# Optimization experiments

Measured on AMD Instinct MI355X. Metric: run time of the kernel, lower is better.

Reference implementation:

```python
import jax, jax.numpy as jnp
import numpy as np

NS = (128, 128, 128)       # ns_mesh
NODES = 4                  # interpolation_nodes (P3M, even -> floor-based indexing)
N_POINTS = 100000
N_CHANNELS = 8
BOX = 10.0


def _weights_p3m4(x):
    # x: (P, 3) relative offsets in [-1/2, 1/2]; returns (4, P, 3)
    x2 = x * x
    x3 = x * x2
    c = jnp.asarray(1.0 / 48.0, dtype=x.dtype)
    return jnp.stack([
        c * (1 - 6 * x + 12 * x2 - 8 * x3),
        c * (23 - 30 * x - 12 * x2 + 24 * x3),
        c * (23 + 30 * x - 12 * x2 - 24 * x3),
        c * (1 + 6 * x + 12 * x2 + 8 * x3),
    ])


def setup_inputs() -> dict:
    key = jax.random.key(0)
    k1, k2 = jax.random.split(key)
    positions = jax.random.uniform(k1, (N_POINTS, 3), dtype=jnp.float32) * BOX
    particle_weights = jax.random.normal(k2, (N_POINTS, N_CHANNELS), dtype=jnp.float32)
    cell = jnp.eye(3, dtype=jnp.float32) * BOX
    return {"positions": positions, "particle_weights": particle_weights, "cell": cell}


def reference(positions, particle_weights, cell):
    nx, ny, nz = NS
    ns_f = jnp.array(NS, dtype=positions.dtype)
    inv_cell = jnp.linalg.inv(cell)

    # --- compute_weights ---
    pos_rel = ns_f * (positions @ inv_cell)        # (P,3) mesh-scaled fractional coords
    idx0 = jnp.floor(pos_rel)                      # even nodes -> floor of position
    offsets = pos_rel - (idx0 + 0.5)               # in [-1/2, 1/2]
    w = _weights_p3m4(offsets)                     # (4, P, 3) per-axis 1d weights
    shifts = jnp.arange(1 - (NODES + 1) // 2, 1 + NODES // 2, dtype=jnp.int32)  # [-1,0,1,2]
    ns_i = jnp.array(NS, dtype=jnp.int32)
    idx = (idx0.astype(jnp.int32)[None] + shifts[:, None, None]) % ns_i  # (4,P,3) periodic
    xi, yi, zi = idx[..., 0], idx[..., 1], idx[..., 2]  # (4,P) each

    # 3D outer product of per-axis weights: (4,4,4,P)
    w3 = w[:, None, None, :, 0] * w[None, :, None, :, 1] * w[None, None, :, :, 2]
    # flattened mesh index per (i,j,k,point): (4,4,4,P)
    lin = (xi[:, None, None] * ny + yi[None, :, None]) * nz + zi[None, None, :]

    # --- points_to_mesh: scatter-add weighted charges onto mesh ---
    C = particle_weights.shape[1]
    vals = w3[..., None] * particle_weights        # (4,4,4,P,C)
    rho_flat = jnp.zeros((nx * ny * nz, C), dtype=positions.dtype)
    rho_flat = rho_flat.at[lin.reshape(-1)].add(vals.reshape(-1, C))

    # --- mesh_to_points: gather mesh values back to particle positions ---
    gathered = rho_flat[lin]                       # (4,4,4,P,C)
    out = jnp.sum(gathered * w3[..., None], axis=(0, 1, 2))  # (P,C)
    return out
```

## Files before the change

### kernel.cpp

```cpp
#include <hip/hip_runtime.h>

static constexpr int NXC   = 128;
static constexpr int NPTS  = 100000;
static constexpr int NCH   = 8;
static constexpr int TS    = 8;
static constexpr int NT    = 16;
static constexpr int NTILES = NT * NT * NT;
static constexpr int NT2   = 32;
static constexpr int NSB   = NT2 * NT2 * NT2;
static constexpr int SLOT2 = 24;
static constexpr int REC   = 20;
static constexpr int SLABCAP = 32;
static constexpr int AMAX  = 14 * SLABCAP;
static constexpr int OMAX2 = 8 * SLOT2;
static constexpr int NMAX  = 48;
static constexpr int NGRP  = 32;

__device__ __forceinline__ void axis_weights(float x, float w[4]) {
    float x2 = x * x, x3 = x2 * x;
    const float c = 1.0f / 48.0f;
    w[0] = c * (1.0f  - 6.0f  * x + 12.0f * x2 - 8.0f  * x3);
    w[1] = c * (23.0f - 30.0f * x - 12.0f * x2 + 24.0f * x3);
    w[2] = c * (23.0f + 30.0f * x - 12.0f * x2 - 24.0f * x3);
    w[3] = c * (1.0f  + 6.0f  * x + 12.0f * x2 + 8.0f  * x3);
}

__device__ __forceinline__ void mesh_coords(const float* __restrict__ pos,
                                            const float* __restrict__ cell,
                                            int p, float& rx, float& ry, float& rz) {
    float a = cell[0], b = cell[1], c = cell[2];
    float d = cell[3], e = cell[4], f = cell[5];
    float g = cell[6], h = cell[7], i9 = cell[8];
    float c00 = e * i9 - f * h, c01 = f * g - d * i9, c02 = d * h - e * g;
    float c10 = c * h - b * i9, c11 = a * i9 - c * g, c12 = b * g - a * h;
    float c20 = b * f - c * e,  c21 = c * d - a * f,  c22 = a * e - b * d;
    float det = a * c00 + b * c01 + c * c02;
    float s = 128.0f / det;
    float p0 = pos[p * 3 + 0], p1 = pos[p * 3 + 1], p2 = pos[p * 3 + 2];
    rx = s * (p0 * c00 + p1 * c01 + p2 * c02);
    ry = s * (p0 * c10 + p1 * c11 + p2 * c12);
    rz = s * (p0 * c20 + p1 * c21 + p2 * c22);
}

__global__ __launch_bounds__(256) void bin_k(const float* __restrict__ pos,
                                             const float* __restrict__ pw,
                                             const float* __restrict__ cell,
                                             int* __restrict__ cursor,
                                             int2* __restrict__ scp,
                                             float* __restrict__ srec) {
    int p = blockIdx.x * 256 + threadIdx.x;
    if (p >= NPTS) return;
    float rx, ry, rz;
    mesh_coords(pos, cell, p, rx, ry, rz);
    float fx = floorf(rx), fy = floorf(ry), fz = floorf(rz);
    int ix = ((int)fx) & (NXC - 1), iy = ((int)fy) & (NXC - 1), iz = ((int)fz) & (NXC - 1);
    int sb = ((ix >> 2) * NT2 + (iy >> 2)) * NT2 + (iz >> 2);
    int slot = atomicAdd(cursor + sb, 1);
    if (slot < SLOT2)
        scp[sb * SLOT2 + slot] = make_int2(ix | (iy << 10) | (iz << 20), p);
    float wx[4], wy[4], wz[4];
    axis_weights(rx - fx - 0.5f, wx);
    axis_weights(ry - fy - 0.5f, wy);
    axis_weights(rz - fz - 0.5f, wz);
    float4* r = reinterpret_cast<float4*>(srec) + (size_t)p * 5;
    r[0] = make_float4(wx[0], wx[1], wx[2], wx[3]);
    r[1] = make_float4(wy[0], wy[1], wy[2], wy[3]);
    r[2] = make_float4(wz[0], wz[1], wz[2], wz[3]);
    const float4* pw4 = reinterpret_cast<const float4*>(pw + (size_t)p * NCH);
    r[3] = pw4[0];
    r[4] = pw4[1];
}

__device__ __forceinline__ float corr4(float4 wp, float4 wq, int d) {
    float s0 = d == 0 ? wq.x : d == -1 ? wq.y : d == -2 ? wq.z : d == -3 ? wq.w : 0.0f;
    float s1 = d == 1 ? wq.x : d ==  0 ? wq.y : d == -1 ? wq.z : d == -2 ? wq.w : 0.0f;
    float s2 = d == 2 ? wq.x : d ==  1 ? wq.y : d ==  0 ? wq.z : d == -1 ? wq.w : 0.0f;
    float s3 = d == 3 ? wq.x : d ==  2 ? wq.y : d ==  1 ? wq.z : d ==  0 ? wq.w : 0.0f;
    return wp.x * s0 + wp.y * s1 + wp.z * s2 + wp.w * s3;
}

__global__ __launch_bounds__(256) void pair_k(const int* __restrict__ cursor,
                                              const int2* __restrict__ scp,
                                              const float* __restrict__ srec,
                                              float* __restrict__ out) {
    __shared__ int2 slab[AMAX];
    __shared__ int2 A12[AMAX];
    __shared__ int nlist[NGRP * NMAX];
    __shared__ int2 own[OMAX2];
    __shared__ int scnt[14];
    __shared__ int soff[15];
    __shared__ int ocnt;

    int b = blockIdx.x;
    int tx = b >> 8, ty = (b >> 4) & 15, tz = b & 15;
    int tid = threadIdx.x;
    int lane = tid & 63;

    if (tid < 14) scnt[tid] = 0;
    if (tid == 0) ocnt = 0;
    __syncthreads();

    {
        int crew = tid >> 2, cl = tid & 3;
        int ox = (crew >> 4) - 1, oy = ((crew >> 2) & 3) - 1, oz = (crew & 3) - 1;
        int sx = (2 * tx + ox) & (NT2 - 1);
        int sy = (2 * ty + oy) & (NT2 - 1);
        int sz = (2 * tz + oz) & (NT2 - 1);
        int sb = (sx * NT2 + sy) * NT2 + sz;
        int n0 = sb * SLOT2;
        int cn = min(cursor[sb], SLOT2);
        bool interior = ((unsigned)ox < 2u) && ((unsigned)oy < 2u) && ((unsigned)oz < 2u);
        int ob = 0;
        if (interior && cl == 0 && cn > 0) ob = atomicAdd(&ocnt, cn);
        ob = __shfl(ob, lane & 60, 64);
        if (interior) {
            for (int s = cl; s < cn; s += 4) own[ob + s] = scp[n0 + s];
        }
        int base_x = tx * TS - 3, base_y = ty * TS - 3, base_z = tz * TS - 3;
        for (int s0 = 0; s0 < cn; s0 += 4) {
            int s = s0 + cl;
            if (s < cn) {
                int2 e = scp[n0 + s];
                int c = e.x;
                int lcx = ((c & 1023) - base_x) & 127;
                int lcy = (((c >> 10) & 1023) - base_y) & 127;
                int lcz = (((c >> 20) & 1023) - base_z) & 127;
                if (lcx < 14 && lcy < 14 && lcz < 14) {
                    int slot = atomicAdd(&scnt[lcx], 1);
                    if (slot < SLABCAP)
                        slab[lcx * SLABCAP + slot] =
                            make_int2(lcy | (lcz << 5) | (lcx << 10), e.y);
                }
            }
        }
    }
    __syncthreads();
    int nown = ocnt;
    if (nown == 0) return;
    if (tid == 0) {
        int run = 0;
        #pragma unroll
        for (int s2 = 0; s2 < 14; ++s2) {
            soff[s2] = run;
            run += min(scnt[s2], SLABCAP);
        }
        soff[14] = run;
    }
    __syncthreads();
    for (int u = tid; u < AMAX; u += 256) {
        int s2 = u >> 5, i2 = u & (SLABCAP - 1);
        if (i2 < min(scnt[s2], SLABCAP)) A12[soff[s2] + i2] = slab[u];
    }
    __syncthreads();

    int sub = tid & 7, pg = tid >> 3;
    const float4* recs = reinterpret_cast<const float4*>(srec);
    int nbl = pg * NMAX;

    for (int p = pg; __any(p < nown); p += NGRP) {
        bool live = p < nown;
        int lpx = 0, lpyh = 0, lpzh = 0, jbeg = 0, span = 0, pid = 0;
        float4 pxw, pyw, pzw;
        if (live) {
            int2 oe = own[p];
            int pc = oe.x;
            pid = oe.y;
            lpx  = (pc & 1023) - tx * TS;
            lpyh = ((pc >> 10) & 1023) - ty * TS + 3;
            lpzh = ((pc >> 20) & 1023) - tz * TS + 3;
            jbeg = soff[lpx];
            span = soff[lpx + 7] - jbeg;
            const float4* r = recs + (size_t)pid * 5;
            pxw = r[0]; pyw = r[1]; pzw = r[2];
        }
        int creg = 0;
        for (int j0 = 0; __any(j0 < span); j0 += 8) {
            bool pass = (j0 + sub) < span;
            int a1 = 0, a2 = 0;
            if (pass) {
                int2 e = A12[jbeg + j0 + sub];
                a1 = e.x; a2 = e.y;
                int dy3 = (a1 & 31) - lpyh + 3;
                int dz3 = ((a1 >> 5) & 31) - lpzh + 3;
                pass = ((unsigned)dy3 <= 6u) && ((unsigned)dz3 <= 6u);
            }
            unsigned long long m = __ballot(pass);
            int mg = (int)(m >> (lane & 56)) & 255;
            if (pass) {
                int slot = creg + __popc(mg & ((1 << sub) - 1));
                if (slot < NMAX) {
                    int dxp3 = ((a1 >> 10) & 15) - lpx;
                    int dy3 = (a1 & 31) - lpyh + 3;
                    int dz3 = ((a1 >> 5) & 31) - lpzh + 3;
                    nlist[nbl + slot] = (a2 << 9) | (dxp3 << 6) | (dy3 << 3) | dz3;
                }
            }
            creg += __popc(mg);
        }
        int n = live ? min(creg, NMAX) : 0;
        float acc[8] = {0, 0, 0, 0, 0, 0, 0, 0};
        for (int s = sub; s < n; s += 8) {
            int ent = nlist[nbl + s];
            const float4* q = recs + (size_t)(ent >> 9) * 5;
            int dx = ((ent >> 6) & 7) - 3;
            int dy = ((ent >> 3) & 7) - 3;
            int dz = (ent & 7) - 3;
            float4 qxw = q[0], qyw = q[1], qzw = q[2];
            float S = corr4(pxw, qxw, dx) * corr4(pyw, qyw, dy) * corr4(pzw, qzw, dz);
            float4 ch0 = q[3], ch1 = q[4];
            acc[0] += S * ch0.x; acc[1] += S * ch0.y;
            acc[2] += S * ch0.z; acc[3] += S * ch0.w;
            acc[4] += S * ch1.x; acc[5] += S * ch1.y;
            acc[6] += S * ch1.z; acc[7] += S * ch1.w;
        }
        float t4[4];
        #pragma unroll
        for (int i = 0; i < 4; ++i) {
            float keep = (sub & 4) ? acc[i + 4] : acc[i];
            float send = (sub & 4) ? acc[i]     : acc[i + 4];
            t4[i] = keep + __shfl_xor(send, 4, 64);
        }
        float t2[2];
        #pragma unroll
        for (int i = 0; i < 2; ++i) {
            float keep = (sub & 2) ? t4[i + 2] : t4[i];
            float send = (sub & 2) ? t4[i]     : t4[i + 2];
            t2[i] = keep + __shfl_xor(send, 2, 64);
        }
        float keep1 = (sub & 1) ? t2[1] : t2[0];
        float send1 = (sub & 1) ? t2[0] : t2[1];
        float rres = keep1 + __shfl_xor(send1, 1, 64);
        if (live) out[(size_t)pid * NCH + sub] = rres;
    }
}

extern "C" void kernel_launch(void* const* d_in, const int* in_sizes, int n_in,
                              void* d_out, int out_size, void* d_ws, size_t ws_size,
                              hipStream_t stream) {
    const float* pos  = (const float*)d_in[0];
    const float* pw   = (const float*)d_in[1];
    const float* cell = (const float*)d_in[2];
    float* out = (float*)d_out;

    int*   cursor = (int*)d_ws;
    int2*  scp    = (int2*)(cursor + NSB);
    float* srec   = (float*)(scp + NSB * SLOT2);

    hipMemsetAsync(cursor, 0, NSB * sizeof(int), stream);

    int pblocks = (NPTS + 255) / 256;
    bin_k<<<pblocks, 256, 0, stream>>>(pos, pw, cell, cursor, scp, srec);
    pair_k<<<NTILES, 256, 0, stream>>>(cursor, scp, srec, out);
}
```

Baseline: 61.00 us.

## Assign one tile per wavefront and build neighbor slab with counting sort

Each 64-lane wavefront now processes its own tile, so a block handles four tiles and the grid shrinks fourfold. The per-x-slice slab-then-compact staging is replaced by a two-pass counting sort: count with shared atomics, take a shuffle prefix scan, then scatter straight into the compact array. Each lane scans a whole sub-box serially instead of four lanes sharing one, and capacity clamps (CMAX, OWNC) are added. This is meant to cut block-wide synchronisation and idle threads on sparse tiles. The cost is serial per-lane loops, two reads of each sub-box and possible truncation if a tile overflows the caps.

```diff
diff --git a/kernel.cpp b/kernel.cpp
--- a/kernel.cpp
+++ b/kernel.cpp
@@ -10,11 +10,9 @@
 static constexpr int NSB   = NT2 * NT2 * NT2;
 static constexpr int SLOT2 = 24;
 static constexpr int REC   = 20;
-static constexpr int SLABCAP = 32;
-static constexpr int AMAX  = 14 * SLABCAP;
-static constexpr int OMAX2 = 8 * SLOT2;
+static constexpr int CMAX  = 224;
+static constexpr int OWNC  = 96;
 static constexpr int NMAX  = 48;
-static constexpr int NGRP  = 32;
 
 __device__ __forceinline__ void axis_weights(float x, float w[4]) {
     float x2 = x * x, x3 = x2 * x;
@@ -83,81 +81,86 @@
                                               const int2* __restrict__ scp,
                                               const float* __restrict__ srec,
                                               float* __restrict__ out) {
-    __shared__ int2 slab[AMAX];
-    __shared__ int2 A12[AMAX];
-    __shared__ int nlist[NGRP * NMAX];
-    __shared__ int2 own[OMAX2];
-    __shared__ int scnt[14];
-    __shared__ int soff[15];
-    __shared__ int ocnt;
-
-    int b = blockIdx.x;
+    __shared__ int2 A12s[4][CMAX];
+    __shared__ int2 owns[4][OWNC];
+    __shared__ int  nlists[4][8 * NMAX];
+    __shared__ int  scnts[4][14];
+    __shared__ int  soffs[4][16];
+    __shared__ int  aoffs[4][14];
+    __shared__ int  ocnts[4];
+
+    int tid = threadIdx.x;
+    int wid = tid >> 6;
+    int lane = tid & 63;
+    int b = blockIdx.x * 4 + wid;
     int tx = b >> 8, ty = (b >> 4) & 15, tz = b & 15;
-    int tid = threadIdx.x;
-    int lane = tid & 63;
-
-    if (tid < 14) scnt[tid] = 0;
-    if (tid == 0) ocnt = 0;
-    __syncthreads();
-
-    {
-        int crew = tid >> 2, cl = tid & 3;
-        int ox = (crew >> 4) - 1, oy = ((crew >> 2) & 3) - 1, oz = (crew & 3) - 1;
-        int sx = (2 * tx + ox) & (NT2 - 1);
-        int sy = (2 * ty + oy) & (NT2 - 1);
-        int sz = (2 * tz + oz) & (NT2 - 1);
-        int sb = (sx * NT2 + sy) * NT2 + sz;
-        int n0 = sb * SLOT2;
-        int cn = min(cursor[sb], SLOT2);
-        bool interior = ((unsigned)ox < 2u) && ((unsigned)oy < 2u) && ((unsigned)oz < 2u);
-        int ob = 0;
-        if (interior && cl == 0 && cn > 0) ob = atomicAdd(&ocnt, cn);
-        ob = __shfl(ob, lane & 60, 64);
-        if (interior) {
-            for (int s = cl; s < cn; s += 4) own[ob + s] = scp[n0 + s];
-        }
-        int base_x = tx * TS - 3, base_y = ty * TS - 3, base_z = tz * TS - 3;
-        for (int s0 = 0; s0 < cn; s0 += 4) {
-            int s = s0 + cl;
-            if (s < cn) {
-                int2 e = scp[n0 + s];
-                int c = e.x;
-                int lcx = ((c & 1023) - base_x) & 127;
-                int lcy = (((c >> 10) & 1023) - base_y) & 127;
-                int lcz = (((c >> 20) & 1023) - base_z) & 127;
-                if (lcx < 14 && lcy < 14 && lcz < 14) {
-                    int slot = atomicAdd(&scnt[lcx], 1);
-                    if (slot < SLABCAP)
-                        slab[lcx * SLABCAP + slot] =
-                            make_int2(lcy | (lcz << 5) | (lcx << 10), e.y);
-                }
-            }
-        }
-    }
-    __syncthreads();
-    int nown = ocnt;
-    if (nown == 0) return;
-    if (tid == 0) {
-        int run = 0;
-        #pragma unroll
-        for (int s2 = 0; s2 < 14; ++s2) {
-            soff[s2] = run;
-            run += min(scnt[s2], SLABCAP);
-        }
-        soff[14] = run;
-    }
-    __syncthreads();
-    for (int u = tid; u < AMAX; u += 256) {
-        int s2 = u >> 5, i2 = u & (SLABCAP - 1);
-        if (i2 < min(scnt[s2], SLABCAP)) A12[soff[s2] + i2] = slab[u];
-    }
-    __syncthreads();
-
-    int sub = tid & 7, pg = tid >> 3;
+
+    int2* A12 = A12s[wid];
+    int2* own = owns[wid];
+    int*  nlist = nlists[wid];
+    int*  scnt = scnts[wid];
+    int*  soff = soffs[wid];
+    int*  aoff = aoffs[wid];
+
+    if (lane < 14) scnt[lane] = 0;
+    if (lane == 0) ocnts[wid] = 0;
+    __syncthreads();
+
+    int ox = (lane >> 4) - 1, oy = ((lane >> 2) & 3) - 1, oz = (lane & 3) - 1;
+    int sx = (2 * tx + ox) & (NT2 - 1);
+    int sy = (2 * ty + oy) & (NT2 - 1);
+    int sz = (2 * tz + oz) & (NT2 - 1);
+    int sb = (sx * NT2 + sy) * NT2 + sz;
+    int n0 = sb * SLOT2;
+    int cn = min(cursor[sb], SLOT2);
+    bool interior = ((unsigned)ox < 2u) && ((unsigned)oy < 2u) && ((unsigned)oz < 2u);
+    int base_x = tx * TS - 3, base_y = ty * TS - 3, base_z = tz * TS - 3;
+
+    int ob = 0;
+    if (interior && cn > 0) ob = atomicAdd(&ocnts[wid], cn);
+    for (int s = 0; s < cn; ++s) {
+        int2 e = scp[n0 + s];
+        if (interior && ob + s < OWNC) own[ob + s] = e;
+        int c = e.x;
+        int lcx = ((c & 1023) - base_x) & 127;
+        int lcy = (((c >> 10) & 1023) - base_y) & 127;
+        int lcz = (((c >> 20) & 1023) - base_z) & 127;
+        if (lcx < 14 && lcy < 14 && lcz < 14) atomicAdd(&scnt[lcx], 1);
+    }
+    __syncthreads();
+
+    int run = (lane < 14) ? scnt[lane] : 0;
+    #pragma unroll
+    for (int d = 1; d < 16; d <<= 1) {
+        int v = __shfl_up(run, d, 16);
+        if ((lane & 15) >= d) run += v;
+    }
+    if (lane == 0) soff[0] = 0;
+    if (lane < 14) soff[lane + 1] = min(run, CMAX);
+    __syncthreads();
+    if (lane < 14) aoff[lane] = soff[lane];
+    __syncthreads();
+
+    for (int s = 0; s < cn; ++s) {
+        int2 e = scp[n0 + s];
+        int c = e.x;
+        int lcx = ((c & 1023) - base_x) & 127;
+        int lcy = (((c >> 10) & 1023) - base_y) & 127;
+        int lcz = (((c >> 20) & 1023) - base_z) & 127;
+        if (lcx < 14 && lcy < 14 && lcz < 14) {
+            int slot = atomicAdd(&aoff[lcx], 1);
+            if (slot < soff[lcx + 1])
+                A12[slot] = make_int2(lcy | (lcz << 5) | (lcx << 10), e.y);
+        }
+    }
+    __syncthreads();
+
+    int nown = min(ocnts[wid], OWNC);
+    int sub = lane & 7, grp = lane >> 3;
     const float4* recs = reinterpret_cast<const float4*>(srec);
-    int nbl = pg * NMAX;
-
-    for (int p = pg; __any(p < nown); p += NGRP) {
+    int nbl = grp * NMAX;
+
+    for (int p = grp; __any(p < nown); p += 8) {
         bool live = p < nown;
         int lpx = 0, lpyh = 0, lpzh = 0, jbeg = 0, span = 0, pid = 0;
         float4 pxw, pyw, pzw;
@@ -165,11 +168,11 @@
             int2 oe = own[p];
             int pc = oe.x;
             pid = oe.y;
-            lpx  = (pc & 1023) - tx * TS;
+            lpx  = ((pc & 1023) - tx * TS) & 7;
             lpyh = ((pc >> 10) & 1023) - ty * TS + 3;
             lpzh = ((pc >> 20) & 1023) - tz * TS + 3;
             jbeg = soff[lpx];
-            span = soff[lpx + 7] - jbeg;
+            span = min(soff[lpx + 7] - jbeg, CMAX);
             const float4* r = recs + (size_t)pid * 5;
             pxw = r[0]; pyw = r[1]; pzw = r[2];
         }
@@ -250,5 +253,5 @@
 
     int pblocks = (NPTS + 255) / 256;
     bin_k<<<pblocks, 256, 0, stream>>>(pos, pw, cell, cursor, scp, srec);
-    pair_k<<<NTILES, 256, 0, stream>>>(cursor, scp, srec, out);
-}
+    pair_k<<<NTILES / 4, 256, 0, stream>>>(cursor, scp, srec, out);
+}
```

Result: slower. 79.92 us (+31.0%).
